# Optimization experiments

Measured on AMD Instinct MI355X. Metric: run time of the kernel, lower is better.

## Reference

```python
import jax, jax.numpy as jnp
import numpy as np

NUM_CLASSES = 1000
FEATURE_DIM = 256
TEMPERATURE = 0.07
EPS = 1e-12  # matches torch F.normalize default eps


def setup_inputs() -> dict:
    key = jax.random.key(0)
    k1, k2, k3, k4 = jax.random.split(key, 4)
    N = 200000
    return {
        "src_feats": jax.random.normal(k1, (N, FEATURE_DIM), dtype=jnp.float32),
        "src_labels": jax.random.randint(k2, (N,), 0, NUM_CLASSES, dtype=jnp.int64),
        "tgt_feats": jax.random.normal(k3, (N, FEATURE_DIM), dtype=jnp.float32),
        "tgt_labels": jax.random.randint(k4, (N,), 0, NUM_CLASSES, dtype=jnp.int64),
    }


def _l2_normalize(x):
    norm = jnp.sqrt(jnp.sum(x * x, axis=1, keepdims=True))
    return x / jnp.maximum(norm, EPS)


def _prototype_init(features, labels):
    """Single-pass segment-mean replacing the per-class python loop.
    prototypes[c] = mean of features with label==c (0 if class absent)."""
    sums = jax.ops.segment_sum(features, labels, num_segments=NUM_CLASSES)  # [C, D]
    counts = jax.ops.segment_sum(jnp.ones_like(labels, dtype=features.dtype),
                                 labels, num_segments=NUM_CLASSES)          # [C]
    protos = sums / jnp.maximum(counts, 1.0)[:, None]
    return protos, counts


def _structure_matrix(protos):
    p = _l2_normalize(protos)
    return p @ p.T  # [C, C]


def reference(src_feats, src_labels, tgt_feats, tgt_labels):
    # PrototypeBank.update with detached features (first call: plain segment-mean)
    src_protos, _ = _prototype_init(jax.lax.stop_gradient(src_feats), src_labels)
    tgt_protos, _ = _prototype_init(jax.lax.stop_gradient(tgt_feats), tgt_labels)

    src_struct = _structure_matrix(src_protos)
    tgt_struct = _structure_matrix(tgt_protos)
    struct_loss = jnp.mean((src_struct - tgt_struct) ** 2)

    # contrastive loss: cosine logits against source prototypes, cross-entropy
    feats_n = _l2_normalize(src_feats)
    protos_n = _l2_normalize(src_protos)
    logits = (feats_n @ protos_n.T) / TEMPERATURE  # [N, C]
    logp = jax.nn.log_softmax(logits, axis=1)
    contrast_loss = -jnp.mean(jnp.take_along_axis(logp, src_labels[:, None], axis=1))

    return struct_loss, contrast_loss, src_protos, src_struct
```

## Files before the change

kernel.cpp:

```cpp
#include <hip/hip_runtime.h>
#include <hip/hip_fp8.h>

#define NCLS 1000
#define DIM 256
#define GCAP 500
#define NT16 64
#define SCLF 20.609930f
#define CP 23.0f
#define CPLN2 15.94238515f
#define LN2 0.69314718056f
#define PADC 2.86102294921875e-06f

typedef __attribute__((ext_vector_type(4))) float f32x4;
typedef long long i64;
typedef unsigned long long u64;

#if defined(__has_builtin) && __has_builtin(__builtin_amdgcn_cvt_pk_fp8_f32)
#define CVTPK(a, b, old, hi) __builtin_amdgcn_cvt_pk_fp8_f32((a), (b), (old), (hi))
#else
__device__ __forceinline__ unsigned cvtpk_sw(float a, float b, unsigned old, bool hi) {
  unsigned lo8 = __hip_cvt_float_to_fp8(a, __HIP_SATFINITE, __HIP_E4M3);
  unsigned hi8 = __hip_cvt_float_to_fp8(b, __HIP_SATFINITE, __HIP_E4M3);
  unsigned pk = lo8 | (hi8 << 8);
  return hi ? ((old & 0xffffu) | (pk << 16)) : ((old & 0xffff0000u) | pk);
}
#define CVTPK(a, b, old, hi) cvtpk_sw((a), (b), (old), (hi))
#endif

__device__ __forceinline__ float fexp2(float x) {
#if __has_builtin(__builtin_amdgcn_exp2f)
  return __builtin_amdgcn_exp2f(x);
#else
  return exp2f(x);
#endif
}

__global__ __launch_bounds__(256) void scatter_kernel(
    const int* __restrict__ sl, const int* __restrict__ tl, int N,
    int* __restrict__ gcnt, int* __restrict__ glist) {
  const int i = blockIdx.x * 256 + threadIdx.x;
  if (i >= 2 * N) return;
  const int side = (i >= N) ? 1 : 0;
  const int r = i - side * N;
  const int c = (side ? tl : sl)[r];
  const int bin = side * NCLS + c;
  const int slot = atomicAdd(gcnt + bin, 1);
  if (slot < GCAP) glist[(size_t)bin * GCAP + slot] = r;
}

__global__ __launch_bounds__(256) void proto_kernel(
    const float* __restrict__ sf, const float* __restrict__ tf,
    const int* __restrict__ gcnt, const int* __restrict__ glist,
    float* __restrict__ mean_out, float* __restrict__ spn, float* __restrict__ tpn,
    unsigned char* __restrict__ pbf8) {
  const int bid = blockIdx.x;
  const int side = (bid < NCLS) ? 1 : 0;
  const int c = side ? bid : (bid - NCLS);
  const int bin = side * NCLS + c;
  const float* feats = side ? tf : sf;
  const int* list = glist + (size_t)bin * GCAP;
  const int m = min(gcnt[bin], GCAP);
  const int t = threadIdx.x;
  const int q = t >> 6, l = t & 63;
  __shared__ float Sp[4][256];
  __shared__ float s_red[4];

  float4 A[8];
  #pragma unroll
  for (int u = 0; u < 8; u++) A[u] = make_float4(0.f, 0.f, 0.f, 0.f);
  int i = q;
  for (; i + 28 < m; i += 32) {
    #pragma unroll
    for (int u = 0; u < 8; u++) {
      const float4 v = *(const float4*)(feats + (size_t)list[i + 4 * u] * DIM + l * 4);
      A[u].x += v.x; A[u].y += v.y; A[u].z += v.z; A[u].w += v.w;
    }
  }
  for (; i < m; i += 4) {
    const float4 v = *(const float4*)(feats + (size_t)list[i] * DIM + l * 4);
    A[0].x += v.x; A[0].y += v.y; A[0].z += v.z; A[0].w += v.w;
  }
  float4 s4;
  s4.x = ((A[0].x + A[1].x) + (A[2].x + A[3].x)) + ((A[4].x + A[5].x) + (A[6].x + A[7].x));
  s4.y = ((A[0].y + A[1].y) + (A[2].y + A[3].y)) + ((A[4].y + A[5].y) + (A[6].y + A[7].y));
  s4.z = ((A[0].z + A[1].z) + (A[2].z + A[3].z)) + ((A[4].z + A[5].z) + (A[6].z + A[7].z));
  s4.w = ((A[0].w + A[1].w) + (A[2].w + A[3].w)) + ((A[4].w + A[5].w) + (A[6].w + A[7].w));
  *(float4*)&Sp[q][l * 4] = s4;
  __syncthreads();

  const float sum = ((Sp[0][t] + Sp[1][t]) + (Sp[2][t] + Sp[3][t]));
  const float mean = sum / fmaxf((float)m, 1.0f);
  if (!side) mean_out[(size_t)c * DIM + t] = mean;

  float ss = mean * mean;
  #pragma unroll
  for (int o = 1; o < 64; o <<= 1) ss += __shfl_xor(ss, o);
  if ((t & 63) == 0) s_red[t >> 6] = ss;
  __syncthreads();
  const float tot = s_red[0] + s_red[1] + s_red[2] + s_red[3];
  const float innv = 1.0f / fmaxf(sqrtf(tot), 1e-12f);
  const float p = mean * innv;
  (side ? tpn : spn)[(size_t)c * DIM + t] = p;
  if (!side) {
    size_t off = (size_t)(c >> 4) * 4096 + (size_t)(t >> 6) * 1024
               + (size_t)((t >> 3) & 3) * 256 + (size_t)(c & 15) * 16
               + (size_t)((t >> 5) & 1) * 8 + (t & 7);
    unsigned qq = CVTPK(p, p, 0u, false);
    pbf8[off] = (unsigned char)(qq & 0xffu);
  }
}

__global__ __launch_bounds__(256, 3) void fused_kernel(
    const float* __restrict__ feats, const int* __restrict__ labels,
    const unsigned char* __restrict__ pbf8, float* __restrict__ accp,
    const float* __restrict__ spn, const float* __restrict__ tpn,
    float* __restrict__ out_struct, float* __restrict__ acc,
    int N, int cblocks) {
  __shared__ __align__(16) unsigned char lds_raw[18432];
  const int bid = blockIdx.x;
  const int t = threadIdx.x;

  if (bid < 256) {
    float (*Sa)[68] = (float(*)[68])(lds_raw);
    float (*Sb)[68] = (float(*)[68])(lds_raw + 4352);
    float (*Ta)[68] = (float(*)[68])(lds_raw + 8704);
    float (*Tb)[68] = (float(*)[68])(lds_raw + 13056);
    float* red = (float*)(lds_raw + 17408);
    const int tx = t & 15, ty = t >> 4;
    const int i0 = (bid >> 4) * 64, j0 = (bid & 15) * 64;
    float cs[4][4], cg[4][4];
    #pragma unroll
    for (int a = 0; a < 4; a++)
      #pragma unroll
      for (int b = 0; b < 4; b++) { cs[a][b] = 0.f; cg[a][b] = 0.f; }

    const int srow = t >> 2;
    const int skq = (t & 3) * 4;
    for (int k0 = 0; k0 < DIM; k0 += 16) {
      __syncthreads();
      {
        float4 z = make_float4(0.f, 0.f, 0.f, 0.f);
        int ra = i0 + srow, rb = j0 + srow;
        float4 va = (ra < NCLS) ? *(const float4*)(spn + (size_t)ra * DIM + k0 + skq) : z;
        float4 vb = (rb < NCLS) ? *(const float4*)(spn + (size_t)rb * DIM + k0 + skq) : z;
        float4 wa = (ra < NCLS) ? *(const float4*)(tpn + (size_t)ra * DIM + k0 + skq) : z;
        float4 wb = (rb < NCLS) ? *(const float4*)(tpn + (size_t)rb * DIM + k0 + skq) : z;
        Sa[skq+0][srow]=va.x; Sa[skq+1][srow]=va.y; Sa[skq+2][srow]=va.z; Sa[skq+3][srow]=va.w;
        Sb[skq+0][srow]=vb.x; Sb[skq+1][srow]=vb.y; Sb[skq+2][srow]=vb.z; Sb[skq+3][srow]=vb.w;
        Ta[skq+0][srow]=wa.x; Ta[skq+1][srow]=wa.y; Ta[skq+2][srow]=wa.z; Ta[skq+3][srow]=wa.w;
        Tb[skq+0][srow]=wb.x; Tb[skq+1][srow]=wb.y; Tb[skq+2][srow]=wb.z; Tb[skq+3][srow]=wb.w;
      }
      __syncthreads();
      #pragma unroll
      for (int k = 0; k < 16; k++) {
        float a[4], b[4], c[4], d[4];
        *(float4*)a = *(const float4*)&Sa[k][ty * 4];
        *(float4*)b = *(const float4*)&Sb[k][tx * 4];
        *(float4*)c = *(const float4*)&Ta[k][ty * 4];
        *(float4*)d = *(const float4*)&Tb[k][tx * 4];
        #pragma unroll
        for (int ii = 0; ii < 4; ii++)
          #pragma unroll
          for (int jj = 0; jj < 4; jj++) {
            cs[ii][jj] = fmaf(a[ii], b[jj], cs[ii][jj]);
            cg[ii][jj] = fmaf(c[ii], d[jj], cg[ii][jj]);
          }
      }
    }
    float d2 = 0.f;
    #pragma unroll
    for (int ii = 0; ii < 4; ii++) {
      int gi = i0 + ty * 4 + ii;
      if (gi < NCLS) {
        #pragma unroll
        for (int jj = 0; jj < 4; jj++) {
          int gj = j0 + tx * 4 + jj;
          if (gj < NCLS) {
            out_struct[(size_t)gi * NCLS + gj] = cs[ii][jj];
            float df = cs[ii][jj] - cg[ii][jj];
            d2 += df * df;
          }
        }
      }
    }
    red[t] = d2;
    __syncthreads();
    for (int o = 128; o > 0; o >>= 1) { if (t < o) red[t] += red[t + o]; __syncthreads(); }
    if (t == 0) atomicAdd(acc, red[0]);
    return;
  }

  const int cbid = bid - 256;
  if (cbid >= cblocks) return;
  const int lane = t & 63;
  const int w = t >> 6;
  const int lx = lane & 15, lg = lane >> 4;
  const int row0 = cbid * 128 + w * 32;
  const float4 z4 = make_float4(0.f, 0.f, 0.f, 0.f);
  const unsigned char* bbase = pbf8 + (lg << 8) + (lx << 4);
  float* Aw = (float*)lds_raw + (size_t)w * (32 * 36);

  i64 af[2][8];
  float sclF[2][4];
  float sSt[2][4];
  int lbR[2];

  float n2a[2] = {0.f, 0.f};
  for (int kc = 0; kc < 8; kc++) {
    #pragma unroll
    for (int i = 0; i < 4; i++) {
      const int f = i * 64 + lane;
      const int row = f >> 3;
      const int c4 = f & 7;
      const int gr = row0 + row;
      float4 v = (gr < N) ? *(const float4*)(feats + (size_t)gr * DIM + kc * 32 + c4 * 4) : z4;
      *(float4*)&Aw[row * 36 + c4 * 4] = v;
    }
    #pragma unroll
    for (int rf = 0; rf < 2; rf++) {
      const int row = rf * 16 + lx;
      float4 x = *(const float4*)&Aw[row * 36 + lg * 8];
      float4 y = *(const float4*)&Aw[row * 36 + lg * 8 + 4];
      n2a[rf] += x.x*x.x + x.y*x.y + x.z*x.z + x.w*x.w
               + y.x*y.x + y.y*y.y + y.z*y.z + y.w*y.w;
      unsigned w0 = CVTPK(x.x, x.y, 0u, false);
      w0 = CVTPK(x.z, x.w, w0, true);
      unsigned w1 = CVTPK(y.x, y.y, 0u, false);
      w1 = CVTPK(y.z, y.w, w1, true);
      af[rf][kc] = (i64)(((u64)w1 << 32) | (u64)w0);
    }
  }
  #pragma unroll
  for (int rf = 0; rf < 2; rf++) {
    const int r = row0 + rf * 16 + lx;
    lbR[rf] = (r < N) ? labels[r] : 0;
    float n2 = n2a[rf];
    n2 += __shfl_xor(n2, 16);
    n2 += __shfl_xor(n2, 32);
    const float sw = SCLF / fmaxf(sqrtf(n2), 1e-12f);
    #pragma unroll
    for (int reg = 0; reg < 4; reg++) {
      sclF[rf][reg] = __shfl(sw, (lg << 2) | reg);
      sSt[rf][reg] = 0.f;
    }
  }

  int4 bA[4], bB[4];

  #define LOADB(dst_, cf_)                                                      \
    {                                                                           \
      const int4* gp = (const int4*)(bbase + ((size_t)(cf_) << 12));            \
      _Pragma("unroll")                                                         \
      for (int q = 0; q < 4; q++) dst_[q] = gp[q << 6];                         \
    }

  #define COMPUTE(buf_)                                                         \
    {                                                                           \
      f32x4 d0 = {0.f, 0.f, 0.f, 0.f};                                          \
      f32x4 d1 = {0.f, 0.f, 0.f, 0.f};                                          \
      _Pragma("unroll")                                                         \
      for (int q = 0; q < 4; q++) {                                             \
        i64 e0 = ((const i64*)&buf_[q])[0];                                     \
        i64 e1 = ((const i64*)&buf_[q])[1];                                     \
        d0 = __builtin_amdgcn_mfma_f32_16x16x32_fp8_fp8(af[0][2*q],   e0, d0, 0, 0, 0); \
        d1 = __builtin_amdgcn_mfma_f32_16x16x32_fp8_fp8(af[1][2*q],   e0, d1, 0, 0, 0); \
        d0 = __builtin_amdgcn_mfma_f32_16x16x32_fp8_fp8(af[0][2*q+1], e1, d0, 0, 0, 0); \
        d1 = __builtin_amdgcn_mfma_f32_16x16x32_fp8_fp8(af[1][2*q+1], e1, d1, 0, 0, 0); \
      }                                                                         \
      _Pragma("unroll")                                                         \
      for (int reg = 0; reg < 4; reg++) {                                       \
        sSt[0][reg] += fexp2(fmaf(d0[reg], sclF[0][reg], -CP));                 \
        sSt[1][reg] += fexp2(fmaf(d1[reg], sclF[1][reg], -CP));                 \
      }                                                                         \
    }

  LOADB(bA, 0);
  for (int cf = 0; cf < NT16; cf += 2) {
    LOADB(bB, cf + 1);
    COMPUTE(bA);
    if (cf + 2 < NT16) LOADB(bA, cf + 2);
    COMPUTE(bB);
  }

  float dvalS[2];
  #pragma unroll
  for (int rf = 0; rf < 2; rf++) {
    const int lb = lbR[rf];
    const unsigned char* gB = pbf8 + ((size_t)(lb >> 4) << 12) + (lg << 8)
                            + ((size_t)(lb & 15) << 4);
    f32x4 dL = {0.f, 0.f, 0.f, 0.f};
    #pragma unroll
    for (int q = 0; q < 4; q++) {
      int4 bg = *(const int4*)(gB + (q << 10));
      i64 e0 = ((const i64*)&bg)[0];
      i64 e1 = ((const i64*)&bg)[1];
      dL = __builtin_amdgcn_mfma_f32_16x16x32_fp8_fp8(af[rf][2*q],   e0, dL, 0, 0, 0);
      dL = __builtin_amdgcn_mfma_f32_16x16x32_fp8_fp8(af[rf][2*q+1], e1, dL, 0, 0, 0);
    }
    const int sel = lx & 3;
    dvalS[rf] = (sel == 0) ? dL[0] : (sel == 1) ? dL[1] : (sel == 2) ? dL[2] : dL[3];
  }

  float wl = 0.f;
  #pragma unroll
  for (int rf = 0; rf < 2; rf++)
    #pragma unroll
    for (int reg = 0; reg < 4; reg++) {
      float s = sSt[rf][reg];
      #pragma unroll
      for (int o = 1; o < 16; o <<= 1) s += __shfl_xor(s, o);
      const int j = (lg << 2) + reg;
      const float lbraw = __shfl(dvalS[rf], ((j >> 2) << 4) | j);
      const int row = row0 + rf * 16 + j;
      if (lx == 0 && row < N)
        wl += logf(s - PADC) + CPLN2 - lbraw * sclF[rf][reg] * LN2;
    }

  #pragma unroll
  for (int o = 1; o < 64; o <<= 1) wl += __shfl_xor(wl, o);
  if (lane == 0) atomicAdd(accp + (cbid & 63), wl);
}

__global__ void final_kernel(const float* __restrict__ acc,
                             const float* __restrict__ accp,
                             float* __restrict__ out, int N) {
  float c = 0.f;
  for (int i = 0; i < 64; i++) c += accp[i];
  out[0] = acc[0] * (1.0f / (float)(NCLS * NCLS));
  out[1] = c / (float)N;
}

extern "C" void kernel_launch(void* const* d_in, const int* in_sizes, int n_in,
                              void* d_out, int out_size, void* d_ws, size_t ws_size,
                              hipStream_t stream) {
  const float* src_feats  = (const float*)d_in[0];
  const int*   src_labels = (const int*)d_in[1];
  const float* tgt_feats  = (const float*)d_in[2];
  const int*   tgt_labels = (const int*)d_in[3];
  const int N = in_sizes[0] / DIM;

  float* ws = (float*)d_ws;
  float* acc    = ws;
  int*   gcnt   = (int*)(ws + 16);
  float* accp   = ws + 2016;
  float* src_pn = ws + 2080;
  float* tgt_pn = ws + 258080;
  unsigned char* pbf8 = (unsigned char*)(ws + 514080);

  float* out_f      = (float*)d_out;
  float* out_protos = out_f + 2;
  float* out_struct = out_f + 2 + NCLS * DIM;
  int* glist = (int*)out_struct;

  hipMemsetAsync(ws, 0, 2080 * sizeof(float), stream);
  hipMemsetAsync(pbf8 + 62 * 4096, 0, 2 * 4096, stream);

  int sblocks = (2 * N + 255) / 256;
  scatter_kernel<<<sblocks, 256, 0, stream>>>(src_labels, tgt_labels, N, gcnt, glist);

  proto_kernel<<<2 * NCLS, 256, 0, stream>>>(src_feats, tgt_feats, gcnt, glist,
                                             out_protos, src_pn, tgt_pn, pbf8);

  int cblocks = (N + 127) / 128;
  fused_kernel<<<256 + cblocks, 256, 0, stream>>>(
      src_feats, src_labels, pbf8, accp, src_pn, tgt_pn, out_struct, acc, N, cblocks);

  final_kernel<<<1, 1, 0, stream>>>(acc, accp, out_f, N);
}
```

Measured before the change: 318.1 us.

## Quantize source rows to fp8 during prototype pass and reuse in fused kernel

The prototype kernel already gathers every source feature row to build the class means. It now also writes an fp8 copy of each row and a per-row inverse-norm scale to workspace. The fused contrastive kernel then loads these precomputed fp8 rows and scales instead of re-reading the fp32 features and doing the norm and conversion itself. This replaces a second full fp32 read of the source features with a smaller fp8 write plus read, at the cost of extra per-row shuffle reductions in the prototype pass. The new path only runs when the workspace is large enough. The fallback path now stages 64-column chunks in a larger LDS buffer. Rows beyond the per-class GCAP cap would never be quantized, so the fast path relies on no class exceeding that cap.

```diff
diff --git a/kernel.cpp b/kernel.cpp
--- a/kernel.cpp
+++ b/kernel.cpp
@@ -52,7 +52,8 @@
     const float* __restrict__ sf, const float* __restrict__ tf,
     const int* __restrict__ gcnt, const int* __restrict__ glist,
     float* __restrict__ mean_out, float* __restrict__ spn, float* __restrict__ tpn,
-    unsigned char* __restrict__ pbf8) {
+    unsigned char* __restrict__ pbf8,
+    float* __restrict__ fscale, unsigned char* __restrict__ ffp8) {
   const int bid = blockIdx.x;
   const int side = (bid < NCLS) ? 1 : 0;
   const int c = side ? bid : (bid - NCLS);
@@ -62,8 +63,20 @@
   const int m = min(gcnt[bin], GCAP);
   const int t = threadIdx.x;
   const int q = t >> 6, l = t & 63;
+  const bool wf8 = (ffp8 != nullptr) && (side == 0);
   __shared__ float Sp[4][256];
   __shared__ float s_red[4];
+
+  #define ROWSIDE(v_, ridx_)                                                    \
+    if (wf8) {                                                                  \
+      float nn = v_.x * v_.x + v_.y * v_.y + v_.z * v_.z + v_.w * v_.w;         \
+      _Pragma("unroll")                                                         \
+      for (int o = 1; o < 64; o <<= 1) nn += __shfl_xor(nn, o);                 \
+      unsigned pk = CVTPK(v_.x, v_.y, 0u, false);                               \
+      pk = CVTPK(v_.z, v_.w, pk, true);                                         \
+      ((unsigned*)(ffp8 + (size_t)(ridx_) * 256))[l] = pk;                      \
+      if (l == 0) fscale[ridx_] = SCLF / fmaxf(sqrtf(nn), 1e-12f);              \
+    }
 
   float4 A[8];
   #pragma unroll
@@ -72,13 +85,17 @@
   for (; i + 28 < m; i += 32) {
     #pragma unroll
     for (int u = 0; u < 8; u++) {
-      const float4 v = *(const float4*)(feats + (size_t)list[i + 4 * u] * DIM + l * 4);
+      const int r = list[i + 4 * u];
+      const float4 v = *(const float4*)(feats + (size_t)r * DIM + l * 4);
       A[u].x += v.x; A[u].y += v.y; A[u].z += v.z; A[u].w += v.w;
+      ROWSIDE(v, r);
     }
   }
   for (; i < m; i += 4) {
-    const float4 v = *(const float4*)(feats + (size_t)list[i] * DIM + l * 4);
+    const int r = list[i];
+    const float4 v = *(const float4*)(feats + (size_t)r * DIM + l * 4);
     A[0].x += v.x; A[0].y += v.y; A[0].z += v.z; A[0].w += v.w;
+    ROWSIDE(v, r);
   }
   float4 s4;
   s4.x = ((A[0].x + A[1].x) + (A[2].x + A[3].x)) + ((A[4].x + A[5].x) + (A[6].x + A[7].x));
@@ -110,13 +127,15 @@
   }
 }
 
+template<int FAST>
 __global__ __launch_bounds__(256, 3) void fused_kernel(
     const float* __restrict__ feats, const int* __restrict__ labels,
     const unsigned char* __restrict__ pbf8, float* __restrict__ accp,
     const float* __restrict__ spn, const float* __restrict__ tpn,
     float* __restrict__ out_struct, float* __restrict__ acc,
+    const unsigned char* __restrict__ ffp8, const float* __restrict__ fscale,
     int N, int cblocks) {
-  __shared__ __align__(16) unsigned char lds_raw[18432];
+  __shared__ __align__(16) unsigned char lds_raw[FAST ? 18432 : 34816];
   const int bid = blockIdx.x;
   const int t = threadIdx.x;
 
@@ -198,50 +217,73 @@
   const int row0 = cbid * 128 + w * 32;
   const float4 z4 = make_float4(0.f, 0.f, 0.f, 0.f);
   const unsigned char* bbase = pbf8 + (lg << 8) + (lx << 4);
-  float* Aw = (float*)lds_raw + (size_t)w * (32 * 36);
 
   i64 af[2][8];
   float sclF[2][4];
   float sSt[2][4];
   int lbR[2];
 
-  float n2a[2] = {0.f, 0.f};
-  for (int kc = 0; kc < 8; kc++) {
-    #pragma unroll
-    for (int i = 0; i < 4; i++) {
-      const int f = i * 64 + lane;
-      const int row = f >> 3;
-      const int c4 = f & 7;
-      const int gr = row0 + row;
-      float4 v = (gr < N) ? *(const float4*)(feats + (size_t)gr * DIM + kc * 32 + c4 * 4) : z4;
-      *(float4*)&Aw[row * 36 + c4 * 4] = v;
-    }
+  if constexpr (FAST) {
     #pragma unroll
     for (int rf = 0; rf < 2; rf++) {
-      const int row = rf * 16 + lx;
-      float4 x = *(const float4*)&Aw[row * 36 + lg * 8];
-      float4 y = *(const float4*)&Aw[row * 36 + lg * 8 + 4];
-      n2a[rf] += x.x*x.x + x.y*x.y + x.z*x.z + x.w*x.w
-               + y.x*y.x + y.y*y.y + y.z*y.z + y.w*y.w;
-      unsigned w0 = CVTPK(x.x, x.y, 0u, false);
-      w0 = CVTPK(x.z, x.w, w0, true);
-      unsigned w1 = CVTPK(y.x, y.y, 0u, false);
-      w1 = CVTPK(y.z, y.w, w1, true);
-      af[rf][kc] = (i64)(((u64)w1 << 32) | (u64)w0);
-    }
-  }
-  #pragma unroll
-  for (int rf = 0; rf < 2; rf++) {
-    const int r = row0 + rf * 16 + lx;
-    lbR[rf] = (r < N) ? labels[r] : 0;
-    float n2 = n2a[rf];
-    n2 += __shfl_xor(n2, 16);
-    n2 += __shfl_xor(n2, 32);
-    const float sw = SCLF / fmaxf(sqrtf(n2), 1e-12f);
-    #pragma unroll
-    for (int reg = 0; reg < 4; reg++) {
-      sclF[rf][reg] = __shfl(sw, (lg << 2) | reg);
-      sSt[rf][reg] = 0.f;
+      const int r = row0 + rf * 16 + lx;
+      const bool v = r < N;
+      const int rc = v ? r : (N - 1);
+      lbR[rf] = v ? labels[r] : 0;
+      const unsigned char* rp8 = ffp8 + (size_t)rc * 256 + (lg << 3);
+      #pragma unroll
+      for (int kc = 0; kc < 8; kc++)
+        af[rf][kc] = v ? *(const i64*)(rp8 + kc * 32) : 0;
+      const float sw = v ? fscale[rc] : 0.f;
+      #pragma unroll
+      for (int reg = 0; reg < 4; reg++) {
+        sclF[rf][reg] = __shfl(sw, (lg << 2) | reg);
+        sSt[rf][reg] = 0.f;
+      }
+    }
+  } else {
+    float* Aw = (float*)lds_raw + (size_t)w * (32 * 68);
+    float n2a[2] = {0.f, 0.f};
+    for (int kc = 0; kc < 4; kc++) {
+      #pragma unroll
+      for (int i = 0; i < 8; i++) {
+        const int f = i * 64 + lane;
+        const int row = f >> 4;
+        const int c4 = f & 15;
+        const int gr = row0 + row;
+        float4 v = (gr < N) ? *(const float4*)(feats + (size_t)gr * DIM + kc * 64 + c4 * 4) : z4;
+        *(float4*)&Aw[row * 68 + c4 * 4] = v;
+      }
+      #pragma unroll
+      for (int rf = 0; rf < 2; rf++) {
+        const int row = rf * 16 + lx;
+        #pragma unroll
+        for (int kk = 0; kk < 2; kk++) {
+          float4 x = *(const float4*)&Aw[row * 68 + kk * 32 + lg * 8];
+          float4 y = *(const float4*)&Aw[row * 68 + kk * 32 + lg * 8 + 4];
+          n2a[rf] += x.x*x.x + x.y*x.y + x.z*x.z + x.w*x.w
+                   + y.x*y.x + y.y*y.y + y.z*y.z + y.w*y.w;
+          unsigned w0 = CVTPK(x.x, x.y, 0u, false);
+          w0 = CVTPK(x.z, x.w, w0, true);
+          unsigned w1 = CVTPK(y.x, y.y, 0u, false);
+          w1 = CVTPK(y.z, y.w, w1, true);
+          af[rf][kc * 2 + kk] = (i64)(((u64)w1 << 32) | (u64)w0);
+        }
+      }
+    }
+    #pragma unroll
+    for (int rf = 0; rf < 2; rf++) {
+      const int r = row0 + rf * 16 + lx;
+      lbR[rf] = (r < N) ? labels[r] : 0;
+      float n2 = n2a[rf];
+      n2 += __shfl_xor(n2, 16);
+      n2 += __shfl_xor(n2, 32);
+      const float sw = SCLF / fmaxf(sqrtf(n2), 1e-12f);
+      #pragma unroll
+      for (int reg = 0; reg < 4; reg++) {
+        sclF[rf][reg] = __shfl(sw, (lg << 2) | reg);
+        sSt[rf][reg] = 0.f;
+      }
     }
   }
 
@@ -346,6 +388,10 @@
   float* src_pn = ws + 2080;
   float* tgt_pn = ws + 258080;
   unsigned char* pbf8 = (unsigned char*)(ws + 514080);
+  float* fscale = ws + 579616;
+  unsigned char* ffp8 = (unsigned char*)(ws + 779616);
+
+  const bool fast = ws_size >= (size_t)56 * 1024 * 1024;
 
   float* out_f      = (float*)d_out;
   float* out_protos = out_f + 2;
@@ -358,12 +404,20 @@
   int sblocks = (2 * N + 255) / 256;
   scatter_kernel<<<sblocks, 256, 0, stream>>>(src_labels, tgt_labels, N, gcnt, glist);
 
-  proto_kernel<<<2 * NCLS, 256, 0, stream>>>(src_feats, tgt_feats, gcnt, glist,
-                                             out_protos, src_pn, tgt_pn, pbf8);
+  proto_kernel<<<2 * NCLS, 256, 0, stream>>>(
+      src_feats, tgt_feats, gcnt, glist, out_protos, src_pn, tgt_pn, pbf8,
+      fast ? fscale : nullptr, fast ? ffp8 : nullptr);
 
   int cblocks = (N + 127) / 128;
-  fused_kernel<<<256 + cblocks, 256, 0, stream>>>(
-      src_feats, src_labels, pbf8, accp, src_pn, tgt_pn, out_struct, acc, N, cblocks);
+  if (fast) {
+    fused_kernel<1><<<256 + cblocks, 256, 0, stream>>>(
+        src_feats, src_labels, pbf8, accp, src_pn, tgt_pn, out_struct, acc,
+        ffp8, fscale, N, cblocks);
+  } else {
+    fused_kernel<0><<<256 + cblocks, 256, 0, stream>>>(
+        src_feats, src_labels, pbf8, accp, src_pn, tgt_pn, out_struct, acc,
+        ffp8, fscale, N, cblocks);
+  }
 
   final_kernel<<<1, 1, 0, stream>>>(acc, accp, out_f, N);
 }
```

After: 347.9 us. 9.4% more time.
